# Performance work log

Hardware: AMD Instinct MI355X
Metric: run time of the kernel (lower is better)

The kernel has to match this reference:

```python
import jax, jax.numpy as jnp
import numpy as np


def setup_inputs() -> dict:
    key = jax.random.key(0)
    inputs = jax.random.normal(key, (8, 4096, 512), dtype=jnp.float32)
    return {"inputs": inputs}


def reference(inputs) -> jnp.ndarray:
    # Faithful math: out = (X @ X^T) @ X  per batch.
    # Expressed via the associativity-equivalent X @ (X^T @ X), which computes
    # the identical result while avoiding the O(S^2) intermediate (S >> D).
    gram = jnp.einsum('bsd,bse->bde', inputs, inputs)   # [B, D, D]
    out = jnp.einsum('bsd,bde->bse', inputs, gram)      # [B, S, D]
    return out
```

## Files before the change

### kernel.cpp

```cpp
#include <hip/hip_runtime.h>
#include <hip/hip_bf16.h>
#include <type_traits>


typedef __attribute__((ext_vector_type(8))) short short8;
typedef __attribute__((ext_vector_type(4))) float floatx4;

#define BM 128
#define BN 128
#define BK 32

#define BATCH 8
#define SEQ 4096
#define DIM 512
#define SPLITK 8

__device__ __forceinline__ void async_copy16(const __hip_bfloat16* g, __hip_bfloat16* l) {
  __builtin_amdgcn_global_load_lds((const __attribute__((address_space(1))) void*)g,
                                   (__attribute__((address_space(3))) void*)l, 16, 0, 0);
}

__global__ __launch_bounds__(256) void transpose_cast_kernel(
    const float* __restrict__ X, __hip_bfloat16* __restrict__ Xt,
    __hip_bfloat16* __restrict__ Xb16) {
  __shared__ float tile[64][65];
  const int b = blockIdx.z;
  const int s0 = blockIdx.x * 64;
  const int d0 = blockIdx.y * 64;
  const int tid = threadIdx.x;
  const float* Xb = X + (long)b * SEQ * DIM;
  __hip_bfloat16* Xtb = Xt + (long)b * DIM * SEQ;
  {
    const int c4 = (tid & 15) * 4;
    const int r0 = tid >> 4;
#pragma unroll
    for (int r = 0; r < 64; r += 16) {
      const float4 v = *(const float4*)&Xb[(long)(s0 + r + r0) * DIM + d0 + c4];
      tile[r + r0][c4 + 0] = v.x;
      tile[r + r0][c4 + 1] = v.y;
      tile[r + r0][c4 + 2] = v.z;
      tile[r + r0][c4 + 3] = v.w;
    }
  }
  __syncthreads();
#pragma unroll
  for (int it = 0; it < 2; ++it) {
    const int idx = it * 256 + tid;
    const int dl = idx >> 3;
    const int so = (idx & 7) * 8;
    union { short8 v; __hip_bfloat16 e[8]; } u;
#pragma unroll
    for (int j = 0; j < 8; ++j) u.e[j] = __float2bfloat16(tile[so + j][dl]);
    *(short8*)&Xtb[(long)(d0 + dl) * SEQ + s0 + so] = u.v;
  }
  if (Xb16 != nullptr) {
    __hip_bfloat16* Xcb = Xb16 + (long)b * SEQ * DIM;
#pragma unroll
    for (int it = 0; it < 2; ++it) {
      const int idx = it * 256 + tid;
      const int sl = idx >> 3;
      const int dc = idx & 7;
      union { short8 v; __hip_bfloat16 e[8]; } u;
#pragma unroll
      for (int j = 0; j < 8; ++j) u.e[j] = __float2bfloat16(tile[sl][dc * 8 + j]);
      *(short8*)&Xcb[(long)(s0 + sl) * DIM + d0 + dc * 8] = u.v;
    }
  }
}

template <int NSPLIT, bool AFP32, int SWZ, typename CT>
__global__ __launch_bounds__(256, 4) void gemm_bt_kernel(
    const float* __restrict__ Af, const __hip_bfloat16* __restrict__ Ab,
    const __hip_bfloat16* __restrict__ Bt, CT* __restrict__ C,
    int K, int lda, int ldb, int ldc, long strideA, long strideB, long strideC) {
  __shared__ __align__(16) __hip_bfloat16 As[2][BM * BK];
  __shared__ __align__(16) __hip_bfloat16 Bs[2][BN * BK];

  int bz, m0, n0;
  if constexpr (SWZ == 1) {
    const int lin = blockIdx.x;
    bz = blockIdx.z;
    const int xcd = lin & 7;
    const int t = lin >> 3;
    n0 = (t & 3) * BN;
    m0 = ((t >> 2) * 8 + xcd) * BM;
  } else if constexpr (SWZ == 2) {
    bz = blockIdx.x;
    const int t = blockIdx.y;
    m0 = (t >> 2) * BM;
    n0 = (t & 3) * BN;
  } else {
    bz = blockIdx.z;
    m0 = blockIdx.y * BM;
    n0 = blockIdx.x * BN;
  }
  const int b = bz / NSPLIT;
  const int split = bz % NSPLIT;
  const int klen = K / NSPLIT;
  const int kb = split * klen;

  const int tid = threadIdx.x;
  const int w = tid >> 6;
  const int lane = tid & 63;
  const int r16 = lane & 15;
  const int kg = lane >> 4;
  const int wr = w >> 1;
  const int wc = w & 1;

  const float* Afb = AFP32 ? Af + b * strideA : nullptr;
  const __hip_bfloat16* Abb = AFP32 ? nullptr : Ab + b * strideA;
  const __hip_bfloat16* Btb = Bt + b * strideB;
  CT* Cb = C + (long)bz * strideC;

  const floatx4 vzero = {0.f, 0.f, 0.f, 0.f};
  floatx4 acc[4][4];
#pragma unroll
  for (int i = 0; i < 4; ++i)
#pragma unroll
    for (int j = 0; j < 4; ++j) acc[i][j] = vzero;

  const int arow = tid >> 1;
  const int ahalf = tid & 1;
  float f[16];

  auto stageB = [&](int buf, int k0) {
#pragma unroll
    for (int q = 0; q < 2; ++q) {
      const __hip_bfloat16* gb =
          Btb + (long)(n0 + w * 32 + q * 16 + (lane >> 2)) * ldb + k0 + (lane & 3) * 8;
      async_copy16(gb, &Bs[buf][(w * 32 + q * 16) * BK]);
    }
  };
  auto stageA = [&](int buf, int k0) {
#pragma unroll
    for (int q = 0; q < 2; ++q) {
      const __hip_bfloat16* ga =
          Abb + (long)(m0 + w * 32 + q * 16 + (lane >> 2)) * lda + k0 + (lane & 3) * 8;
      async_copy16(ga, &As[buf][(w * 32 + q * 16) * BK]);
    }
  };
  auto loadF = [&](int k0) {
    const float* ar = Afb + (long)(m0 + arow) * lda + k0 + ahalf * 16;
    *(float4*)(f + 0)  = *(const float4*)(ar + 0);
    *(float4*)(f + 4)  = *(const float4*)(ar + 4);
    *(float4*)(f + 8)  = *(const float4*)(ar + 8);
    *(float4*)(f + 12) = *(const float4*)(ar + 12);
  };
  auto writeF = [&](int buf) {
    union { short8 v[2]; __hip_bfloat16 e[16]; } u;
#pragma unroll
    for (int t = 0; t < 16; ++t) u.e[t] = __float2bfloat16(f[t]);
    short8* dst = (short8*)&As[buf][arow * BK + ahalf * 16];
    dst[0] = u.v[0];
    dst[1] = u.v[1];
  };

  const int nIter = klen / BK;
  if constexpr (AFP32) {
    loadF(kb);
    writeF(0);
    loadF(kb + BK);
  } else {
    stageA(0, kb);
  }
  stageB(0, kb);

  for (int t = 0; t < nIter; ++t) {
    const int cur = t & 1;
    __syncthreads();
    if (t + 1 < nIter) {
      if constexpr (AFP32) {
        writeF(cur ^ 1);
        if (t + 2 < nIter) loadF(kb + (t + 2) * BK);
      } else {
        stageA(cur ^ 1, kb + (t + 1) * BK);
      }
      stageB(cur ^ 1, kb + (t + 1) * BK);
    }

    short8 a[4], bfrag[4];
#pragma unroll
    for (int i = 0; i < 4; ++i)
      a[i] = *(const short8*)&As[cur][(wr * 64 + i * 16 + r16) * BK + kg * 8];
#pragma unroll
    for (int j = 0; j < 4; ++j)
      bfrag[j] = *(const short8*)&Bs[cur][(wc * 64 + j * 16 + r16) * BK + kg * 8];
#pragma unroll
    for (int i = 0; i < 4; ++i)
#pragma unroll
      for (int j = 0; j < 4; ++j)
        acc[i][j] = __builtin_amdgcn_mfma_f32_16x16x32_bf16(a[i], bfrag[j], acc[i][j], 0, 0, 0);
  }

#pragma unroll
  for (int i = 0; i < 4; ++i) {
    const int row_base = m0 + wr * 64 + i * 16 + kg * 4;
#pragma unroll
    for (int j = 0; j < 4; ++j) {
      const int col = n0 + wc * 64 + j * 16 + r16;
#pragma unroll
      for (int r = 0; r < 4; ++r) {
        const float v = acc[i][j][r];
        if constexpr (std::is_same<CT, float>::value)
          Cb[(long)(row_base + r) * ldc + col] = v;
        else
          Cb[(long)(row_base + r) * ldc + col] = __float2bfloat16(v);
      }
    }
  }
}

template <int NSPLIT>
__global__ __launch_bounds__(256) void reduce_cast_kernel(
    const __hip_bfloat16* __restrict__ P, __hip_bfloat16* __restrict__ G) {
  const int DD8 = DIM * DIM / 8;
  const long idx = (long)blockIdx.x * 256 + threadIdx.x;
  const int b = (int)(idx / DD8);
  const int e = (int)(idx % DD8);
  const __hip_bfloat16* base = P + (long)(b * NSPLIT) * DIM * DIM + (long)e * 8;
  float s[8] = {0.f, 0.f, 0.f, 0.f, 0.f, 0.f, 0.f, 0.f};
#pragma unroll
  for (int p = 0; p < NSPLIT; ++p) {
    union { short8 v; __hip_bfloat16 e8[8]; } u;
    u.v = *(const short8*)(base + (long)p * DIM * DIM);
#pragma unroll
    for (int j = 0; j < 8; ++j) s[j] += __bfloat162float(u.e8[j]);
  }
  union { short8 v; __hip_bfloat16 e8[8]; } o;
#pragma unroll
  for (int j = 0; j < 8; ++j) o.e8[j] = __float2bfloat16(s[j]);
  *(short8*)&G[(long)idx * 8] = o.v;
}

extern "C" void kernel_launch(void* const* d_in, const int* in_sizes, int n_in,
                              void* d_out, int out_size, void* d_ws, size_t ws_size,
                              hipStream_t stream) {
  const float* X = (const float*)d_in[0];
  float* out = (float*)d_out;
  const long xtBytes = (long)BATCH * DIM * SEQ * 2;
  const long gramBytes = (long)BATCH * DIM * DIM * 2;
  const long partBytes = (long)BATCH * SPLITK * DIM * DIM * 2;
  __hip_bfloat16* Xt = (__hip_bfloat16*)d_out;
  __hip_bfloat16* gram = (__hip_bfloat16*)d_ws;

  const bool bigWs = ws_size >= (size_t)(gramBytes + xtBytes + partBytes);
  const bool midWs = ws_size >= (size_t)(gramBytes + xtBytes);
  __hip_bfloat16* Xb16 = midWs ? (__hip_bfloat16*)((char*)d_ws + gramBytes) : nullptr;

  transpose_cast_kernel<<<dim3(SEQ / 64, DIM / 64, BATCH), 256, 0, stream>>>(X, Xt, Xb16);

  __hip_bfloat16* partials = bigWs
      ? (__hip_bfloat16*)((char*)d_ws + gramBytes + xtBytes)
      : (__hip_bfloat16*)((char*)d_out + xtBytes);
  gemm_bt_kernel<SPLITK, false, 2, __hip_bfloat16>
      <<<dim3(BATCH * SPLITK, 16, 1), 256, 0, stream>>>(
          nullptr, Xt, Xt, partials, SEQ, SEQ, SEQ, DIM,
          (long)DIM * SEQ, (long)DIM * SEQ, (long)DIM * DIM);
  reduce_cast_kernel<SPLITK><<<dim3(BATCH * DIM * DIM / 8 / 256), 256, 0, stream>>>(
      partials, gram);

  if (midWs) {
    gemm_bt_kernel<1, false, 1, float><<<dim3(128, 1, BATCH), 256, 0, stream>>>(
        nullptr, Xb16, gram, out, DIM, DIM, DIM, DIM,
        (long)SEQ * DIM, (long)DIM * DIM, (long)SEQ * DIM);
  } else {
    gemm_bt_kernel<1, true, 1, float><<<dim3(128, 1, BATCH), 256, 0, stream>>>(
        X, nullptr, gram, out, DIM, DIM, DIM, DIM,
        (long)SEQ * DIM, (long)DIM * DIM, (long)SEQ * DIM);
  }
}
```

Measured before the change: 168.5 us.

## Exploit Gram symmetry: compute upper-triangle tiles and mirror in reduction

The Gram matrix X^T X is symmetric, so the split-K GEMM now launches only the 10 upper-triangular 128x128 tiles per batch instead of 16. The reduce kernel sums the partials per tile and writes both the tile and, through an LDS transpose, its mirror. This removes about 37% of the Gram GEMM FLOPs and partial traffic. In exchange the reduce grid is far smaller (80 blocks) and does more work per block, which may limit its parallelism.

```diff
diff --git a/kernel.cpp b/kernel.cpp
--- a/kernel.cpp
+++ b/kernel.cpp
@@ -18,6 +18,13 @@
 __device__ __forceinline__ void async_copy16(const __hip_bfloat16* g, __hip_bfloat16* l) {
   __builtin_amdgcn_global_load_lds((const __attribute__((address_space(1))) void*)g,
                                    (__attribute__((address_space(3))) void*)l, 16, 0, 0);
+}
+
+__device__ __forceinline__ void tri_map(int t, int& ti, int& tj) {
+  if (t < 4)      { ti = 0; tj = t; }
+  else if (t < 7) { ti = 1; tj = t - 3; }
+  else if (t < 9) { ti = 2; tj = t - 5; }
+  else            { ti = 3; tj = 3; }
 }
 
 __global__ __launch_bounds__(256) void transpose_cast_kernel(
@@ -86,9 +93,10 @@
     m0 = ((t >> 2) * 8 + xcd) * BM;
   } else if constexpr (SWZ == 2) {
     bz = blockIdx.x;
-    const int t = blockIdx.y;
-    m0 = (t >> 2) * BM;
-    n0 = (t & 3) * BN;
+    int ti, tj;
+    tri_map(blockIdx.y, ti, tj);
+    m0 = ti * BM;
+    n0 = tj * BN;
   } else {
     bz = blockIdx.z;
     m0 = blockIdx.y * BM;
@@ -211,25 +219,62 @@
 }
 
 template <int NSPLIT>
-__global__ __launch_bounds__(256) void reduce_cast_kernel(
+__global__ __launch_bounds__(256) void reduce_mirror_kernel(
     const __hip_bfloat16* __restrict__ P, __hip_bfloat16* __restrict__ G) {
-  const int DD8 = DIM * DIM / 8;
-  const long idx = (long)blockIdx.x * 256 + threadIdx.x;
-  const int b = (int)(idx / DD8);
-  const int e = (int)(idx % DD8);
-  const __hip_bfloat16* base = P + (long)(b * NSPLIT) * DIM * DIM + (long)e * 8;
-  float s[8] = {0.f, 0.f, 0.f, 0.f, 0.f, 0.f, 0.f, 0.f};
-#pragma unroll
-  for (int p = 0; p < NSPLIT; ++p) {
-    union { short8 v; __hip_bfloat16 e8[8]; } u;
-    u.v = *(const short8*)(base + (long)p * DIM * DIM);
-#pragma unroll
-    for (int j = 0; j < 8; ++j) s[j] += __bfloat162float(u.e8[j]);
-  }
-  union { short8 v; __hip_bfloat16 e8[8]; } o;
-#pragma unroll
-  for (int j = 0; j < 8; ++j) o.e8[j] = __float2bfloat16(s[j]);
-  *(short8*)&G[(long)idx * 8] = o.v;
+  __shared__ float tile[64][65];
+  int ti, tj;
+  tri_map(blockIdx.x, ti, tj);
+  const int b = blockIdx.y;
+  const __hip_bfloat16* Pb = P + (long)b * NSPLIT * DIM * DIM;
+  __hip_bfloat16* Gb = G + (long)b * DIM * DIM;
+  const int r0 = ti * 128, c0 = tj * 128;
+  const int tid = threadIdx.x;
+  const int lrow = tid >> 3;
+  const int lcol = (tid & 7) * 8;
+
+#pragma unroll
+  for (int q = 0; q < 4; ++q) {
+    const int qr = (q >> 1) * 64, qc = (q & 1) * 64;
+    float s[2][8];
+#pragma unroll
+    for (int h = 0; h < 2; ++h) {
+      const int row = lrow + h * 32;
+#pragma unroll
+      for (int j = 0; j < 8; ++j) s[h][j] = 0.f;
+#pragma unroll
+      for (int p = 0; p < NSPLIT; ++p) {
+        union { short8 v; __hip_bfloat16 e8[8]; } u;
+        u.v = *(const short8*)&Pb[(long)p * DIM * DIM +
+                                  (long)(r0 + qr + row) * DIM + c0 + qc + lcol];
+#pragma unroll
+        for (int j = 0; j < 8; ++j) s[h][j] += __bfloat162float(u.e8[j]);
+      }
+      union { short8 v; __hip_bfloat16 e8[8]; } o;
+#pragma unroll
+      for (int j = 0; j < 8; ++j) o.e8[j] = __float2bfloat16(s[h][j]);
+      *(short8*)&Gb[(long)(r0 + qr + row) * DIM + c0 + qc + lcol] = o.v;
+    }
+    if (ti != tj) {
+      if (q) __syncthreads();
+#pragma unroll
+      for (int h = 0; h < 2; ++h) {
+        const int row = lrow + h * 32;
+#pragma unroll
+        for (int j = 0; j < 8; ++j) tile[row][lcol + j] = s[h][j];
+      }
+      __syncthreads();
+#pragma unroll
+      for (int it = 0; it < 2; ++it) {
+        const int idx = it * 256 + tid;
+        const int dl = idx >> 3;
+        const int so = (idx & 7) * 8;
+        union { short8 v; __hip_bfloat16 e8[8]; } o;
+#pragma unroll
+        for (int j = 0; j < 8; ++j) o.e8[j] = __float2bfloat16(tile[so + j][dl]);
+        *(short8*)&Gb[(long)(c0 + qc + dl) * DIM + r0 + qr + so] = o.v;
+      }
+    }
+  }
 }
 
 extern "C" void kernel_launch(void* const* d_in, const int* in_sizes, int n_in,
@@ -253,11 +298,11 @@
       ? (__hip_bfloat16*)((char*)d_ws + gramBytes + xtBytes)
       : (__hip_bfloat16*)((char*)d_out + xtBytes);
   gemm_bt_kernel<SPLITK, false, 2, __hip_bfloat16>
-      <<<dim3(BATCH * SPLITK, 16, 1), 256, 0, stream>>>(
+      <<<dim3(BATCH * SPLITK, 10, 1), 256, 0, stream>>>(
           nullptr, Xt, Xt, partials, SEQ, SEQ, SEQ, DIM,
           (long)DIM * SEQ, (long)DIM * SEQ, (long)DIM * DIM);
-  reduce_cast_kernel<SPLITK><<<dim3(BATCH * DIM * DIM / 8 / 256), 256, 0, stream>>>(
-      partials, gram);
+
+  reduce_mirror_kernel<SPLITK><<<dim3(10, BATCH), 256, 0, stream>>>(partials, gram);
 
   if (midWs) {
     gemm_bt_kernel<1, false, 1, float><<<dim3(128, 1, BATCH), 256, 0, stream>>>(
```

After: 166.8 us. No clear change (-1.0%).
